# Optimization experiments

Measured on AMD Instinct MI355X. Metric: run time of the kernel, lower is better.

Reference implementation:

```python
import jax, jax.numpy as jnp
import numpy as np

# dataset / mesh constants (from ds_props)
NX_PATCH, NY_PATCH = 10, 6       # Nx_patch * Ny_patch == 60 (hardcoded N_patch)
PX = 16                          # patch_size == out_patch_size
NPX, NPY = NX_PATCH * PX, NY_PATCH * PX
N_NODES = NPX * NPY              # 15360
HID = 128


def make_edge_idx(n, m):
    """Bidirectional 4-neighbor grid edges; n rows, m cols; node idx = j*n + i."""
    jj, ii = np.meshgrid(np.arange(m), np.arange(n - 1), indexing='ij')
    a = (jj * n + ii).ravel()
    e_v = np.concatenate([np.stack([a, a + 1]), np.stack([a + 1, a])], axis=1)
    ii2, jj2 = np.meshgrid(np.arange(n), np.arange(m - 1), indexing='ij')
    b = (jj2 * n + ii2).ravel()
    e_h = np.concatenate([np.stack([b, b + n]), np.stack([b + n, b])], axis=1)
    return np.concatenate([e_v, e_h], axis=1).astype(np.int32)  # [2, E]


def setup_inputs() -> dict:
    key = jax.random.key(0)
    ks = jax.random.split(key, 6)
    bs, seq_len, in_dim = 4, 32, 1024
    s = 0.02
    return {
        'patch_vectors': jax.random.normal(ks[0], (bs, seq_len * 60, in_dim), jnp.float32),
        'W1': jax.random.normal(ks[1], (in_dim, 512), jnp.float32) * s,
        'b1': jnp.zeros((512,), jnp.float32),
        'W2': jax.random.normal(ks[2], (512, HID), jnp.float32) * s,
        'b2': jnp.zeros((HID,), jnp.float32),
        'Wg': jax.random.normal(ks[3], (HID + 4, 3), jnp.float32) * s,
        'bg': jnp.zeros((3,), jnp.float32),
        'edge_index': jnp.asarray(make_edge_idx(NPY, NPX)),  # make_edge_idx(Ny_mesh, Nx_mesh)
    }


def _coord_feats():
    # patch index per pixel: (Npx, Npy, 2), raw integer patch coords (as in source)
    xg, yg = jnp.meshgrid(jnp.arange(NX_PATCH), jnp.arange(NY_PATCH), indexing='ij')
    pidx = jnp.stack([xg, yg], axis=-1).astype(jnp.float32)          # (Nx_patch, Ny_patch, 2)
    pidx = jnp.repeat(jnp.repeat(pidx, PX, axis=0), PX, axis=1)       # (Npx, Npy, 2)
    # pixel index within patch, normalized by global max (px-1), tiled over patches
    xp, yp = jnp.meshgrid(jnp.arange(PX), jnp.arange(PX), indexing='ij')
    pix = jnp.stack([xp, yp], axis=-1).astype(jnp.float32) / (PX - 1)
    pix = jnp.tile(pix, (NX_PATCH, NY_PATCH, 1))                      # (Npx, Npy, 2)
    return pidx, pix


def reference(patch_vectors, W1, b1, W2, b2, Wg, bg, edge_index):
    bs, tot_patchs, _ = patch_vectors.shape
    seq_len = tot_patchs // 60
    # input MLP: Linear -> softplus -> Linear
    h = jax.nn.softplus(patch_vectors @ W1 + b1) @ W2 + b2            # (bs, tot, 128)
    h = h.reshape(bs, seq_len, NX_PATCH, NY_PATCH, HID)
    # patch_to_px: repeat_interleave upsample to pixel mesh
    h = jnp.repeat(jnp.repeat(h, PX, axis=2), PX, axis=3)             # (bs, seq, Npx, Npy, 128)
    pidx, pix = _coord_feats()
    pidx = jnp.broadcast_to(pidx, (bs, seq_len, NPX, NPY, 2))
    pix = jnp.broadcast_to(pix, (bs, seq_len, NPX, NPY, 2))
    feat = jnp.concatenate([h, pidx, pix], axis=-1)                   # (..., 132)
    feat = feat.reshape(bs * seq_len, N_NODES, HID + 4)               # (B, N, 132)
    # GCNConv with self-loops: D^{-1/2} (A+I) D^{-1/2} X W + b
    src, dst = edge_index[0], edge_index[1]
    deg = 1.0 + jax.ops.segment_sum(jnp.ones(src.shape, jnp.float32), dst, num_segments=N_NODES)
    dinv = jax.lax.rsqrt(deg)
    norm = dinv[src] * dinv[dst]                                      # (E,)
    xw = feat @ Wg                                                    # (B, N, 3)
    agg = jax.vmap(lambda m: jax.ops.segment_sum(m, dst, num_segments=N_NODES))(
        xw[:, src, :] * norm[None, :, None])                          # scatter-add over edges
    out = agg + xw * (1.0 / deg)[None, :, None] + bg                  # self-loop term + bias
    return out.reshape(-1, NPX, NPY, 3)
```

## Files before the change

kernel.cpp:

```cpp
#include <hip/hip_runtime.h>
#include <math.h>

typedef __bf16 bf16_t;
typedef __bf16 bf16x8 __attribute__((ext_vector_type(8)));
typedef float f32x4 __attribute__((ext_vector_type(4)));

#define M_ROWS 7680
#define N1 512
#define K1 1024
#define NPX 160
#define NPY 96
#define BDIM 128
#define NPATCH 60
#define NPIX (BDIM*NPX*NPY)

#define OFF_WGEFF   0
#define OFF_BIASEFF 1536
#define OFF_CF      2048
#define OFF_HW      48128
#define OFF_HWPART  71168
#define OFF_W1T     255488

#define BM 64
#define BN 64
#define BK 64
#define LDT 72

__global__ __launch_bounds__(256) void prep_kernel(
    const float* __restrict__ W1, const float* __restrict__ W2,
    const float* __restrict__ b2, const float* __restrict__ Wg,
    const float* __restrict__ bg, float* __restrict__ ws)
{
    const int t = threadIdx.x;
    if (blockIdx.x < 128) {
        __shared__ bf16_t tile[64][72];
        const int k0 = (blockIdx.x & 15) * 64;
        const int n0 = (blockIdx.x >> 4) * 64;
        bf16_t* W1T = (bf16_t*)(ws + OFF_W1T);
#pragma unroll
        for (int i = 0; i < 4; ++i) {
            int idx = t + i * 256;
            int r = idx >> 4, ch = idx & 15;
            float4 v = *(const float4*)(W1 + (size_t)(k0 + r) * N1 + n0 + ch * 4);
            bf16_t* dst = &tile[r][ch * 4];
            dst[0] = (bf16_t)v.x; dst[1] = (bf16_t)v.y;
            dst[2] = (bf16_t)v.z; dst[3] = (bf16_t)v.w;
        }
        __syncthreads();
#pragma unroll
        for (int i = 0; i < 2; ++i) {
            int idx = t + i * 256;
            int nr = idx >> 3, kc = idx & 7;
            bf16x8 o;
#pragma unroll
            for (int j = 0; j < 8; ++j) o[j] = tile[kc * 8 + j][nr];
            *(bf16x8*)(W1T + (size_t)(n0 + nr) * K1 + k0 + kc * 8) = o;
        }
    } else if (blockIdx.x == 128) {
#pragma unroll
        for (int rep = 0; rep < 2; ++rep) {
            int j = t + rep * 256;
            float a0 = 0.f, a1 = 0.f, a2 = 0.f;
            for (int k = 0; k < 128; ++k) {
                float w = W2[j * 128 + k];
                a0 = fmaf(w, Wg[k * 3 + 0], a0);
                a1 = fmaf(w, Wg[k * 3 + 1], a1);
                a2 = fmaf(w, Wg[k * 3 + 2], a2);
            }
            ws[OFF_WGEFF + j * 3 + 0] = a0;
            ws[OFF_WGEFF + j * 3 + 1] = a1;
            ws[OFF_WGEFF + j * 3 + 2] = a2;
        }
        if (t < 3) {
            float s = 0.f;
            for (int k = 0; k < 128; ++k) s = fmaf(b2[k], Wg[k * 3 + t], s);
            ws[OFF_BIASEFF + t] = s;
        }
    } else {
        int e = (blockIdx.x - 129) * 256 + t;
        int c = e % 3;
        int p = e / 3;
        int x = p / NPY, y = p % NPY;
        float wpx = Wg[128 * 3 + c], wpy = Wg[129 * 3 + c];
        float wqx = Wg[130 * 3 + c], wqy = Wg[131 * 3 + c];
        auto aff = [&](int xx, int yy) -> float {
            return (float)(xx >> 4) * wpx + (float)(yy >> 4) * wpy
                 + (float)(xx & 15) * (1.f / 15.f) * wqx
                 + (float)(yy & 15) * (1.f / 15.f) * wqy;
        };
        auto deg = [&](int xx, int yy) -> float {
            return 1.f + (xx > 0) + (xx < NPX - 1) + (yy > 0) + (yy < NPY - 1);
        };
        float degc = deg(x, y);
        float s = 0.f;
        if (x > 0)       s += rsqrtf(deg(x - 1, y)) * aff(x - 1, y);
        if (x < NPX - 1) s += rsqrtf(deg(x + 1, y)) * aff(x + 1, y);
        if (y > 0)       s += rsqrtf(deg(x, y - 1)) * aff(x, y - 1);
        if (y < NPY - 1) s += rsqrtf(deg(x, y + 1)) * aff(x, y + 1);
        ws[OFF_CF + e] = rsqrtf(degc) * s + aff(x, y) / degc + bg[c];
    }
}

static __device__ inline bf16x8 cvt8(float4 a, float4 b) {
    bf16x8 v;
    v[0] = (bf16_t)a.x; v[1] = (bf16_t)a.y; v[2] = (bf16_t)a.z; v[3] = (bf16_t)a.w;
    v[4] = (bf16_t)b.x; v[5] = (bf16_t)b.y; v[6] = (bf16_t)b.z; v[7] = (bf16_t)b.w;
    return v;
}

__global__ __launch_bounds__(256, 4) void gemm_mfma_kernel(
    const float* __restrict__ A,
    const float* __restrict__ b1,
    const float* __restrict__ ws,
    float* __restrict__ hw_part)
{
    __shared__ __align__(16) char smem[36864];
    bf16_t* sA = (bf16_t*)smem;
    bf16_t* sB = sA + 2 * BM * LDT;
    float* red = (float*)smem;
    const bf16_t* W1T = (const bf16_t*)(ws + OFF_W1T);

    const int bid = blockIdx.x;
    const int xcd = bid & 7;
    const int local = bid >> 3;
    const int nblk = local & 7;
    const int mblk = xcd * 15 + (local >> 3);
    const int m0 = mblk * BM;
    const int n0 = nblk * BN;

    const int t = threadIdx.x;
    const int lane = t & 63;
    const int wv = t >> 6;
    const int wr = wv >> 1, wc = wv & 1;
    const int l15 = lane & 15, hi = lane >> 4;

    const int srow = t >> 2;
    const int sq = (t & 3) << 4;
    const float*  aptr = A   + (size_t)(m0 + srow) * K1 + sq;
    const bf16_t* bptr = W1T + (size_t)(n0 + srow) * K1 + sq;
    const int swoff = srow * LDT + sq;

    f32x4 acc[2][2];
#pragma unroll
    for (int i = 0; i < 2; ++i)
#pragma unroll
        for (int j = 0; j < 2; ++j) acc[i][j] = (f32x4)0.f;

    {
        float4 fa0 = *(const float4*)(aptr + 0);
        float4 fa1 = *(const float4*)(aptr + 4);
        float4 fa2 = *(const float4*)(aptr + 8);
        float4 fa3 = *(const float4*)(aptr + 12);
        uint4  ub0 = *(const uint4*)(bptr);
        uint4  ub1 = *(const uint4*)(bptr + 8);
        *(bf16x8*)(sA + swoff)     = cvt8(fa0, fa1);
        *(bf16x8*)(sA + swoff + 8) = cvt8(fa2, fa3);
        *(uint4*)(sB + swoff)      = ub0;
        *(uint4*)(sB + swoff + 8)  = ub1;
    }
    __syncthreads();

    int cur = 0;
    for (int ks = 0; ks < K1 / BK; ++ks) {
        float4 fa0, fa1, fa2, fa3; uint4 ub0, ub1;
        const bool pf = (ks < K1 / BK - 1);
        if (pf) {
            const float*  ap = aptr + (ks + 1) * BK;
            const bf16_t* bp = bptr + (ks + 1) * BK;
            fa0 = *(const float4*)(ap + 0);
            fa1 = *(const float4*)(ap + 4);
            fa2 = *(const float4*)(ap + 8);
            fa3 = *(const float4*)(ap + 12);
            ub0 = *(const uint4*)(bp);
            ub1 = *(const uint4*)(bp + 8);
        }
        const bf16_t* cA = sA + cur * (BM * LDT);
        const bf16_t* cB = sB + cur * (BM * LDT);
        bf16x8 af[2][2], bfr[2][2];
#pragma unroll
        for (int i = 0; i < 2; ++i)
#pragma unroll
            for (int kk = 0; kk < 2; ++kk) {
                af[i][kk]  = *(const bf16x8*)(cA + (wr * 32 + i * 16 + l15) * LDT + kk * 32 + hi * 8);
                bfr[i][kk] = *(const bf16x8*)(cB + (wc * 32 + i * 16 + l15) * LDT + kk * 32 + hi * 8);
            }
#pragma unroll
        for (int kk = 0; kk < 2; ++kk)
#pragma unroll
            for (int mi = 0; mi < 2; ++mi)
#pragma unroll
                for (int ni = 0; ni < 2; ++ni)
                    acc[mi][ni] = __builtin_amdgcn_mfma_f32_16x16x32_bf16(
                        af[mi][kk], bfr[ni][kk], acc[mi][ni], 0, 0, 0);
        if (pf) {
            bf16_t* nA = sA + (cur ^ 1) * (BM * LDT);
            bf16_t* nB = sB + (cur ^ 1) * (BM * LDT);
            *(bf16x8*)(nA + swoff)     = cvt8(fa0, fa1);
            *(bf16x8*)(nA + swoff + 8) = cvt8(fa2, fa3);
            *(uint4*)(nB + swoff)      = ub0;
            *(uint4*)(nB + swoff + 8)  = ub1;
        }
        __syncthreads();
        cur ^= 1;
    }

    float b1v[2], wgv[2][3];
#pragma unroll
    for (int ni = 0; ni < 2; ++ni) {
        int n = n0 + wc * 32 + ni * 16 + l15;
        b1v[ni]    = b1[n];
        wgv[ni][0] = ws[OFF_WGEFF + n * 3 + 0];
        wgv[ni][1] = ws[OFF_WGEFF + n * 3 + 1];
        wgv[ni][2] = ws[OFF_WGEFF + n * 3 + 2];
    }
#pragma unroll
    for (int mi = 0; mi < 2; ++mi)
#pragma unroll
        for (int r = 0; r < 4; ++r) {
            float p0 = 0.f, p1 = 0.f, p2 = 0.f;
#pragma unroll
            for (int ni = 0; ni < 2; ++ni) {
                float z = acc[mi][ni][r] + b1v[ni];
                float sp = fmaxf(z, 0.f) + __logf(1.f + __expf(-fabsf(z)));
                p0 = fmaf(sp, wgv[ni][0], p0);
                p1 = fmaf(sp, wgv[ni][1], p1);
                p2 = fmaf(sp, wgv[ni][2], p2);
            }
            int ml = wr * 32 + mi * 16 + hi * 4 + r;
            int j  = wc * 16 + l15;
            float* dst = red + (ml * 32 + j) * 3;
            dst[0] = p0; dst[1] = p1; dst[2] = p2;
        }
    __syncthreads();
    if (t < 192) {
        int m = t / 3, c = t - m * 3;
        float s = 0.f;
#pragma unroll
        for (int j = 0; j < 32; ++j) s += red[(m * 32 + j) * 3 + c];
        hw_part[((size_t)nblk * M_ROWS + m0 + m) * 3 + c] = s;
    }
}

__global__ __launch_bounds__(256) void reduce_kernel(float* __restrict__ ws)
{
    int idx = blockIdx.x * 256 + threadIdx.x;
    if (idx >= M_ROWS * 3) return;
    int c = idx % 3;
    float s = ws[OFF_BIASEFF + c];
#pragma unroll
    for (int jb = 0; jb < 8; ++jb) s += ws[OFF_HWPART + jb * M_ROWS * 3 + idx];
    ws[OFF_HW + idx] = s;
}

__global__ __launch_bounds__(256) void stencil_kernel(
    const float* __restrict__ ws, float* __restrict__ out)
{
    int tid = blockIdx.x * 256 + threadIdx.x;
    int p0 = tid * 4;
    int b = p0 / (NPX * NPY);
    int rem = p0 - b * (NPX * NPY);
    int x = rem / NPY, y0 = rem - x * NPY;

    const float* hwb = ws + OFF_HW + b * NPATCH * 3;
    const float* cf = ws + OFF_CF;

    auto deg = [&](int xx, int yy) -> float {
        return 1.f + (xx > 0) + (xx < NPX - 1) + (yy > 0) + (yy < NPY - 1);
    };
    auto hwp = [&](int xx, int yy) -> const float* {
        return hwb + ((xx >> 4) * 6 + (yy >> 4)) * 3;
    };

    float res[4][3];
#pragma unroll
    for (int i = 0; i < 4; ++i) {
        int y = y0 + i;
        float degc = deg(x, y);
        float dinvc = rsqrtf(degc);
        float s0 = 0.f, s1 = 0.f, s2 = 0.f;
        auto tap = [&](int xx, int yy) {
            float dn = rsqrtf(deg(xx, yy));
            const float* h = hwp(xx, yy);
            s0 = fmaf(dn, h[0], s0);
            s1 = fmaf(dn, h[1], s1);
            s2 = fmaf(dn, h[2], s2);
        };
        if (x > 0)       tap(x - 1, y);
        if (x < NPX - 1) tap(x + 1, y);
        if (y > 0)       tap(x, y - 1);
        if (y < NPY - 1) tap(x, y + 1);
        const float* hs = hwp(x, y);
        const float* c = cf + (x * NPY + y) * 3;
        float inv_deg = 1.f / degc;
        res[i][0] = c[0] + fmaf(dinvc, s0, hs[0] * inv_deg);
        res[i][1] = c[1] + fmaf(dinvc, s1, hs[1] * inv_deg);
        res[i][2] = c[2] + fmaf(dinvc, s2, hs[2] * inv_deg);
    }
    float4 v0 = {res[0][0], res[0][1], res[0][2], res[1][0]};
    float4 v1 = {res[1][1], res[1][2], res[2][0], res[2][1]};
    float4 v2 = {res[2][2], res[3][0], res[3][1], res[3][2]};
    float* o = out + (size_t)p0 * 3;
    *(float4*)(o + 0) = v0;
    *(float4*)(o + 4) = v1;
    *(float4*)(o + 8) = v2;
}

extern "C" void kernel_launch(void* const* d_in, const int* in_sizes, int n_in,
                              void* d_out, int out_size, void* d_ws, size_t ws_size,
                              hipStream_t stream) {
    const float* pv = (const float*)d_in[0];
    const float* W1 = (const float*)d_in[1];
    const float* b1 = (const float*)d_in[2];
    const float* W2 = (const float*)d_in[3];
    const float* b2 = (const float*)d_in[4];
    const float* Wg = (const float*)d_in[5];
    const float* bg = (const float*)d_in[6];

    float* ws = (float*)d_ws;
    float* out = (float*)d_out;

    hipLaunchKernelGGL(prep_kernel, dim3(309), dim3(256), 0, stream,
                       W1, W2, b2, Wg, bg, ws);
    hipLaunchKernelGGL(gemm_mfma_kernel, dim3(960), dim3(256), 0, stream,
                       pv, b1, ws, ws + OFF_HWPART);
    hipLaunchKernelGGL(reduce_kernel, dim3(90), dim3(256), 0, stream,
                       ws);
    hipLaunchKernelGGL(stencil_kernel, dim3(NPIX / 4 / 256), dim3(256), 0, stream,
                       ws, out);
}
```

Before: 61.87 us.

## Split GEMM tile across eight waves with 512-thread blocks

Doubles the GEMM block from 256 to 512 threads (eight waves), so each wave computes a 32x16 sub-tile instead of 32x32, and each thread loads half as much per K step. The epilogue is rewritten to reduce the two column-halves through shared memory in two phases. The aim is more waves in flight to hide global load latency. The cost is extra barriers, redundant A-fragment LDS reads, and smaller MFMA work per wave.

```diff
diff --git a/kernel.cpp b/kernel.cpp
--- a/kernel.cpp
+++ b/kernel.cpp
@@ -108,7 +108,7 @@
     return v;
 }
 
-__global__ __launch_bounds__(256, 4) void gemm_mfma_kernel(
+__global__ __launch_bounds__(512, 8) void gemm_mfma_kernel(
     const float* __restrict__ A,
     const float* __restrict__ b1,
     const float* __restrict__ ws,
@@ -131,106 +131,105 @@
     const int t = threadIdx.x;
     const int lane = t & 63;
     const int wv = t >> 6;
-    const int wr = wv >> 1, wc = wv & 1;
+    const int wr = wv & 1;
+    const int wcn = wv >> 1;
     const int l15 = lane & 15, hi = lane >> 4;
 
-    const int srow = t >> 2;
-    const int sq = (t & 3) << 4;
-    const float*  aptr = A   + (size_t)(m0 + srow) * K1 + sq;
-    const bf16_t* bptr = W1T + (size_t)(n0 + srow) * K1 + sq;
-    const int swoff = srow * LDT + sq;
-
-    f32x4 acc[2][2];
-#pragma unroll
-    for (int i = 0; i < 2; ++i)
-#pragma unroll
-        for (int j = 0; j < 2; ++j) acc[i][j] = (f32x4)0.f;
+    const int srow = t >> 3;
+    const int oct = (t & 7) << 3;
+    const float*  aptr = A   + (size_t)(m0 + srow) * K1 + oct;
+    const bf16_t* bptr = W1T + (size_t)(n0 + srow) * K1 + oct;
+    const int swoff = srow * LDT + oct;
+
+    f32x4 acc[2];
+    acc[0] = (f32x4)0.f; acc[1] = (f32x4)0.f;
 
     {
         float4 fa0 = *(const float4*)(aptr + 0);
         float4 fa1 = *(const float4*)(aptr + 4);
-        float4 fa2 = *(const float4*)(aptr + 8);
-        float4 fa3 = *(const float4*)(aptr + 12);
         uint4  ub0 = *(const uint4*)(bptr);
-        uint4  ub1 = *(const uint4*)(bptr + 8);
-        *(bf16x8*)(sA + swoff)     = cvt8(fa0, fa1);
-        *(bf16x8*)(sA + swoff + 8) = cvt8(fa2, fa3);
-        *(uint4*)(sB + swoff)      = ub0;
-        *(uint4*)(sB + swoff + 8)  = ub1;
+        *(bf16x8*)(sA + swoff) = cvt8(fa0, fa1);
+        *(uint4*)(sB + swoff)  = ub0;
     }
     __syncthreads();
 
     int cur = 0;
     for (int ks = 0; ks < K1 / BK; ++ks) {
-        float4 fa0, fa1, fa2, fa3; uint4 ub0, ub1;
+        float4 fa0, fa1; uint4 ub0;
         const bool pf = (ks < K1 / BK - 1);
         if (pf) {
             const float*  ap = aptr + (ks + 1) * BK;
             const bf16_t* bp = bptr + (ks + 1) * BK;
             fa0 = *(const float4*)(ap + 0);
             fa1 = *(const float4*)(ap + 4);
-            fa2 = *(const float4*)(ap + 8);
-            fa3 = *(const float4*)(ap + 12);
             ub0 = *(const uint4*)(bp);
-            ub1 = *(const uint4*)(bp + 8);
         }
         const bf16_t* cA = sA + cur * (BM * LDT);
         const bf16_t* cB = sB + cur * (BM * LDT);
-        bf16x8 af[2][2], bfr[2][2];
-#pragma unroll
-        for (int i = 0; i < 2; ++i)
-#pragma unroll
-            for (int kk = 0; kk < 2; ++kk) {
-                af[i][kk]  = *(const bf16x8*)(cA + (wr * 32 + i * 16 + l15) * LDT + kk * 32 + hi * 8);
-                bfr[i][kk] = *(const bf16x8*)(cB + (wc * 32 + i * 16 + l15) * LDT + kk * 32 + hi * 8);
-            }
+        bf16x8 af[2][2], bfr[2];
+#pragma unroll
+        for (int kk = 0; kk < 2; ++kk) {
+#pragma unroll
+            for (int mi = 0; mi < 2; ++mi)
+                af[mi][kk] = *(const bf16x8*)(cA + (wr * 32 + mi * 16 + l15) * LDT + kk * 32 + hi * 8);
+            bfr[kk] = *(const bf16x8*)(cB + (wcn * 16 + l15) * LDT + kk * 32 + hi * 8);
+        }
 #pragma unroll
         for (int kk = 0; kk < 2; ++kk)
 #pragma unroll
             for (int mi = 0; mi < 2; ++mi)
-#pragma unroll
-                for (int ni = 0; ni < 2; ++ni)
-                    acc[mi][ni] = __builtin_amdgcn_mfma_f32_16x16x32_bf16(
-                        af[mi][kk], bfr[ni][kk], acc[mi][ni], 0, 0, 0);
+                acc[mi] = __builtin_amdgcn_mfma_f32_16x16x32_bf16(
+                    af[mi][kk], bfr[kk], acc[mi], 0, 0, 0);
         if (pf) {
             bf16_t* nA = sA + (cur ^ 1) * (BM * LDT);
             bf16_t* nB = sB + (cur ^ 1) * (BM * LDT);
-            *(bf16x8*)(nA + swoff)     = cvt8(fa0, fa1);
-            *(bf16x8*)(nA + swoff + 8) = cvt8(fa2, fa3);
-            *(uint4*)(nB + swoff)      = ub0;
-            *(uint4*)(nB + swoff + 8)  = ub1;
+            *(bf16x8*)(nA + swoff) = cvt8(fa0, fa1);
+            *(uint4*)(nB + swoff)  = ub0;
         }
         __syncthreads();
         cur ^= 1;
     }
 
-    float b1v[2], wgv[2][3];
-#pragma unroll
-    for (int ni = 0; ni < 2; ++ni) {
-        int n = n0 + wc * 32 + ni * 16 + l15;
-        b1v[ni]    = b1[n];
-        wgv[ni][0] = ws[OFF_WGEFF + n * 3 + 0];
-        wgv[ni][1] = ws[OFF_WGEFF + n * 3 + 1];
-        wgv[ni][2] = ws[OFF_WGEFF + n * 3 + 2];
-    }
+    const int n = n0 + wcn * 16 + l15;
+    const float bb = b1[n];
+    const float wg0 = ws[OFF_WGEFF + n * 3 + 0];
+    const float wg1 = ws[OFF_WGEFF + n * 3 + 1];
+    const float wg2 = ws[OFF_WGEFF + n * 3 + 2];
+    const int jslot = (wcn & 1) * 16 + l15;
+
+    float p[2][4][3];
 #pragma unroll
     for (int mi = 0; mi < 2; ++mi)
 #pragma unroll
         for (int r = 0; r < 4; ++r) {
-            float p0 = 0.f, p1 = 0.f, p2 = 0.f;
-#pragma unroll
-            for (int ni = 0; ni < 2; ++ni) {
-                float z = acc[mi][ni][r] + b1v[ni];
-                float sp = fmaxf(z, 0.f) + __logf(1.f + __expf(-fabsf(z)));
-                p0 = fmaf(sp, wgv[ni][0], p0);
-                p1 = fmaf(sp, wgv[ni][1], p1);
-                p2 = fmaf(sp, wgv[ni][2], p2);
+            float z = acc[mi][r] + bb;
+            float sp = fmaxf(z, 0.f) + __logf(1.f + __expf(-fabsf(z)));
+            p[mi][r][0] = sp * wg0;
+            p[mi][r][1] = sp * wg1;
+            p[mi][r][2] = sp * wg2;
+        }
+    __syncthreads();
+    if (wcn < 2) {
+#pragma unroll
+        for (int mi = 0; mi < 2; ++mi)
+#pragma unroll
+            for (int r = 0; r < 4; ++r) {
+                int ml = wr * 32 + mi * 16 + hi * 4 + r;
+                float* dst = red + (ml * 32 + jslot) * 3;
+                dst[0] = p[mi][r][0]; dst[1] = p[mi][r][1]; dst[2] = p[mi][r][2];
             }
-            int ml = wr * 32 + mi * 16 + hi * 4 + r;
-            int j  = wc * 16 + l15;
-            float* dst = red + (ml * 32 + j) * 3;
-            dst[0] = p0; dst[1] = p1; dst[2] = p2;
-        }
+    }
+    __syncthreads();
+    if (wcn >= 2) {
+#pragma unroll
+        for (int mi = 0; mi < 2; ++mi)
+#pragma unroll
+            for (int r = 0; r < 4; ++r) {
+                int ml = wr * 32 + mi * 16 + hi * 4 + r;
+                float* dst = red + (ml * 32 + jslot) * 3;
+                dst[0] += p[mi][r][0]; dst[1] += p[mi][r][1]; dst[2] += p[mi][r][2];
+            }
+    }
     __syncthreads();
     if (t < 192) {
         int m = t / 3, c = t - m * 3;
@@ -321,7 +320,7 @@
 
     hipLaunchKernelGGL(prep_kernel, dim3(309), dim3(256), 0, stream,
                        W1, W2, b2, Wg, bg, ws);
-    hipLaunchKernelGGL(gemm_mfma_kernel, dim3(960), dim3(256), 0, stream,
+    hipLaunchKernelGGL(gemm_mfma_kernel, dim3(960), dim3(512), 0, stream,
                        pv, b1, ws, ws + OFF_HWPART);
     hipLaunchKernelGGL(reduce_kernel, dim3(90), dim3(256), 0, stream,
                        ws);
```

After: 59.78 us. -3.4%, faster.

## Load GEMM B fragments directly to registers and fuse partial reduce into stencil

Applied to the files above, without the earlier changes.

The GEMM now loads W1T fragments straight from global memory into registers, software-pipelined one K-step ahead, instead of staging them through shared memory. This shrinks LDS use and removes the B-tile LDS writes and reads, at the cost of more registers and uncoalesced global reads, and the occupancy hint is dropped. The separate reduce kernel is removed. Each stencil block (one batch, one patch column of 16 x-rows) now sums the 8 partials for its neighbouring patches into shared memory itself, which saves a launch and a global round trip.

```diff
diff --git a/kernel.cpp b/kernel.cpp
--- a/kernel.cpp
+++ b/kernel.cpp
@@ -108,15 +108,14 @@
     return v;
 }
 
-__global__ __launch_bounds__(256, 4) void gemm_mfma_kernel(
+__global__ __launch_bounds__(256) void gemm_mfma_kernel(
     const float* __restrict__ A,
     const float* __restrict__ b1,
     const float* __restrict__ ws,
     float* __restrict__ hw_part)
 {
-    __shared__ __align__(16) char smem[36864];
+    __shared__ __align__(16) char smem[24576];
     bf16_t* sA = (bf16_t*)smem;
-    bf16_t* sB = sA + 2 * BM * LDT;
     float* red = (float*)smem;
     const bf16_t* W1T = (const bf16_t*)(ws + OFF_W1T);
 
@@ -136,9 +135,10 @@
 
     const int srow = t >> 2;
     const int sq = (t & 3) << 4;
-    const float*  aptr = A   + (size_t)(m0 + srow) * K1 + sq;
-    const bf16_t* bptr = W1T + (size_t)(n0 + srow) * K1 + sq;
+    const float* aptr = A + (size_t)(m0 + srow) * K1 + sq;
     const int swoff = srow * LDT + sq;
+
+    const bf16_t* bbase = W1T + (size_t)(n0 + wc * 32 + l15) * K1 + hi * 8;
 
     f32x4 acc[2][2];
 #pragma unroll
@@ -151,39 +151,42 @@
         float4 fa1 = *(const float4*)(aptr + 4);
         float4 fa2 = *(const float4*)(aptr + 8);
         float4 fa3 = *(const float4*)(aptr + 12);
-        uint4  ub0 = *(const uint4*)(bptr);
-        uint4  ub1 = *(const uint4*)(bptr + 8);
         *(bf16x8*)(sA + swoff)     = cvt8(fa0, fa1);
         *(bf16x8*)(sA + swoff + 8) = cvt8(fa2, fa3);
-        *(uint4*)(sB + swoff)      = ub0;
-        *(uint4*)(sB + swoff + 8)  = ub1;
-    }
+    }
+    bf16x8 bcur[2][2];
+#pragma unroll
+    for (int ni = 0; ni < 2; ++ni)
+#pragma unroll
+        for (int kk = 0; kk < 2; ++kk)
+            bcur[ni][kk] = *(const bf16x8*)(bbase + (size_t)ni * 16 * K1 + kk * 32);
     __syncthreads();
 
     int cur = 0;
     for (int ks = 0; ks < K1 / BK; ++ks) {
-        float4 fa0, fa1, fa2, fa3; uint4 ub0, ub1;
+        float4 fa0, fa1, fa2, fa3;
+        bf16x8 bnext[2][2];
         const bool pf = (ks < K1 / BK - 1);
         if (pf) {
-            const float*  ap = aptr + (ks + 1) * BK;
-            const bf16_t* bp = bptr + (ks + 1) * BK;
+            const float* ap = aptr + (ks + 1) * BK;
             fa0 = *(const float4*)(ap + 0);
             fa1 = *(const float4*)(ap + 4);
             fa2 = *(const float4*)(ap + 8);
             fa3 = *(const float4*)(ap + 12);
-            ub0 = *(const uint4*)(bp);
-            ub1 = *(const uint4*)(bp + 8);
+            const bf16_t* bp = bbase + (ks + 1) * BK;
+#pragma unroll
+            for (int ni = 0; ni < 2; ++ni)
+#pragma unroll
+                for (int kk = 0; kk < 2; ++kk)
+                    bnext[ni][kk] = *(const bf16x8*)(bp + (size_t)ni * 16 * K1 + kk * 32);
         }
         const bf16_t* cA = sA + cur * (BM * LDT);
-        const bf16_t* cB = sB + cur * (BM * LDT);
-        bf16x8 af[2][2], bfr[2][2];
-#pragma unroll
-        for (int i = 0; i < 2; ++i)
-#pragma unroll
-            for (int kk = 0; kk < 2; ++kk) {
-                af[i][kk]  = *(const bf16x8*)(cA + (wr * 32 + i * 16 + l15) * LDT + kk * 32 + hi * 8);
-                bfr[i][kk] = *(const bf16x8*)(cB + (wc * 32 + i * 16 + l15) * LDT + kk * 32 + hi * 8);
-            }
+        bf16x8 af[2][2];
+#pragma unroll
+        for (int mi = 0; mi < 2; ++mi)
+#pragma unroll
+            for (int kk = 0; kk < 2; ++kk)
+                af[mi][kk] = *(const bf16x8*)(cA + (wr * 32 + mi * 16 + l15) * LDT + kk * 32 + hi * 8);
 #pragma unroll
         for (int kk = 0; kk < 2; ++kk)
 #pragma unroll
@@ -191,14 +194,16 @@
 #pragma unroll
                 for (int ni = 0; ni < 2; ++ni)
                     acc[mi][ni] = __builtin_amdgcn_mfma_f32_16x16x32_bf16(
-                        af[mi][kk], bfr[ni][kk], acc[mi][ni], 0, 0, 0);
+                        af[mi][kk], bcur[ni][kk], acc[mi][ni], 0, 0, 0);
         if (pf) {
             bf16_t* nA = sA + (cur ^ 1) * (BM * LDT);
-            bf16_t* nB = sB + (cur ^ 1) * (BM * LDT);
             *(bf16x8*)(nA + swoff)     = cvt8(fa0, fa1);
             *(bf16x8*)(nA + swoff + 8) = cvt8(fa2, fa3);
-            *(uint4*)(nB + swoff)      = ub0;
-            *(uint4*)(nB + swoff + 8)  = ub1;
+#pragma unroll
+            for (int ni = 0; ni < 2; ++ni)
+#pragma unroll
+                for (int kk = 0; kk < 2; ++kk)
+                    bcur[ni][kk] = bnext[ni][kk];
         }
         __syncthreads();
         cur ^= 1;
@@ -241,34 +246,42 @@
     }
 }
 
-__global__ __launch_bounds__(256) void reduce_kernel(float* __restrict__ ws)
-{
-    int idx = blockIdx.x * 256 + threadIdx.x;
-    if (idx >= M_ROWS * 3) return;
-    int c = idx % 3;
-    float s = ws[OFF_BIASEFF + c];
-#pragma unroll
-    for (int jb = 0; jb < 8; ++jb) s += ws[OFF_HWPART + jb * M_ROWS * 3 + idx];
-    ws[OFF_HW + idx] = s;
-}
-
-__global__ __launch_bounds__(256) void stencil_kernel(
+__global__ __launch_bounds__(384) void stencil_kernel(
     const float* __restrict__ ws, float* __restrict__ out)
 {
-    int tid = blockIdx.x * 256 + threadIdx.x;
-    int p0 = tid * 4;
-    int b = p0 / (NPX * NPY);
-    int rem = p0 - b * (NPX * NPY);
-    int x = rem / NPY, y0 = rem - x * NPY;
-
-    const float* hwb = ws + OFF_HW + b * NPATCH * 3;
+    __shared__ float hwl[3][6][3];
+    const int blk = blockIdx.x;
+    const int b = blk / 10;
+    const int px0 = blk % 10;
+    const int x0 = px0 * 16;
+    const int t = threadIdx.x;
+
+    if (t < 54) {
+        int j = t / 3, c = t - (t / 3) * 3;
+        int dxi = j / 6, py = j % 6;
+        int px = px0 - 1 + dxi;
+        float v = 0.f;
+        if (px >= 0 && px < 10) {
+            int m = b * NPATCH + px * 6 + py;
+            v = ws[OFF_BIASEFF + c];
+#pragma unroll
+            for (int s = 0; s < 8; ++s)
+                v += ws[OFF_HWPART + ((size_t)s * M_ROWS + m) * 3 + c];
+        }
+        hwl[dxi][py][c] = v;
+    }
+    __syncthreads();
+
+    const int xr = t / 24;
+    const int y0 = (t - xr * 24) * 4;
+    const int x = x0 + xr;
     const float* cf = ws + OFF_CF;
 
     auto deg = [&](int xx, int yy) -> float {
         return 1.f + (xx > 0) + (xx < NPX - 1) + (yy > 0) + (yy < NPY - 1);
     };
     auto hwp = [&](int xx, int yy) -> const float* {
-        return hwb + ((xx >> 4) * 6 + (yy >> 4)) * 3;
+        return &hwl[(xx >> 4) - (px0 - 1)][yy >> 4][0];
     };
 
     float res[4][3];
@@ -299,7 +312,8 @@
     float4 v0 = {res[0][0], res[0][1], res[0][2], res[1][0]};
     float4 v1 = {res[1][1], res[1][2], res[2][0], res[2][1]};
     float4 v2 = {res[2][2], res[3][0], res[3][1], res[3][2]};
-    float* o = out + (size_t)p0 * 3;
+    size_t p0 = ((size_t)b * NPX + x) * NPY + y0;
+    float* o = out + p0 * 3;
     *(float4*)(o + 0) = v0;
     *(float4*)(o + 4) = v1;
     *(float4*)(o + 8) = v2;
@@ -323,8 +337,6 @@
                        W1, W2, b2, Wg, bg, ws);
     hipLaunchKernelGGL(gemm_mfma_kernel, dim3(960), dim3(256), 0, stream,
                        pv, b1, ws, ws + OFF_HWPART);
-    hipLaunchKernelGGL(reduce_kernel, dim3(90), dim3(256), 0, stream,
-                       ws);
-    hipLaunchKernelGGL(stencil_kernel, dim3(NPIX / 4 / 256), dim3(256), 0, stream,
+    hipLaunchKernelGGL(stencil_kernel, dim3(1280), dim3(384), 0, stream,
                        ws, out);
 }
```

Measured after the change: 77.69 us. 1.26x slower.
